# Kernel optimization log

Measured on AMD Instinct MI355X. Metric: run time of the kernel, lower is better.

## Reference

```python
import jax, jax.numpy as jnp
import numpy as np

DATA = 2048   # data_size / hidden_size
WIDTH = 4096  # width_size
T = 1000      # len(ts)


def setup_inputs() -> dict:
    key = jax.random.key(0)
    ks = jax.random.split(key, 10)
    # ts: evenly spaced times; small dt keeps 1000 Euler steps stable
    ts = jnp.arange(T, dtype=jnp.float32) * 1e-3
    y0 = jax.random.normal(ks[0], (DATA,), dtype=jnp.float32)
    def lin(k, fan_out, fan_in):
        kw, kb = jax.random.split(k)
        s = 1.0 / np.sqrt(fan_in)
        W = jax.random.uniform(kw, (fan_out, fan_in), jnp.float32, -s, s)
        b = jax.random.uniform(kb, (fan_out,), jnp.float32, -s, s)
        return W, b
    # eqx.nn.MLP(depth=3): in->w, w->w, w->w, w->out, softplus on all but last
    W0, b0 = lin(ks[1], WIDTH, DATA)
    W1, b1 = lin(ks[2], WIDTH, WIDTH)
    W2, b2 = lin(ks[3], WIDTH, WIDTH)
    W3, b3 = lin(ks[4], DATA, WIDTH)
    return {"ts": ts, "y0": y0, "W0": W0, "b0": b0, "W1": W1, "b1": b1,
            "W2": W2, "b2": b2, "W3": W3, "b3": b3}


def reference(ts, y0, W0, b0, W1, b1, W2, b2, W3, b3):
    dt = ts[1] - ts[0]

    def mlp(y):
        h = jax.nn.softplus(W0 @ y + b0)
        h = jax.nn.softplus(W1 @ h + b1)
        h = jax.nn.softplus(W2 @ h + b2)
        return W3 @ h + b3

    def step(y, _):
        y1 = y + dt * mlp(y)  # Euler step: y + dt * f(t, y)
        return y1, y1

    _, ys = jax.lax.scan(step, y0, None, length=ts.shape[0])
    return ys  # [T, DATA]
```

## Files before the change

### kernel.cpp

```cpp
#include <hip/hip_runtime.h>

#define NWG   256
#define TPB_R 256
#define TPB_S 1024
#define NSTEP 1000
#define NDATA 2048
#define WIDTH 4096

typedef __attribute__((ext_vector_type(4))) float f32x4;
typedef __attribute__((ext_vector_type(2))) float f32x2;
typedef __attribute__((ext_vector_type(2))) unsigned int u32x2;
typedef __attribute__((ext_vector_type(4))) unsigned int u32x4;
typedef unsigned int uint;

#define SCHED_FENCE() __builtin_amdgcn_sched_barrier(0)


__device__ __forceinline__ float sp_f(float v) {
  return fmaxf(v, 0.0f) + log1pf(expf(-fabsf(v)));
}

__device__ __forceinline__ float wred(float v) {
#pragma unroll
  for (int m = 32; m > 0; m >>= 1) v += __shfl_xor(v, m, 64);
  return v;
}


__device__ __forceinline__ void wait_vm0()   { asm volatile("s_waitcnt vmcnt(0)" ::: "memory"); SCHED_FENCE(); }
template<int N>
__device__ __forceinline__ void wait_vmN()   { asm volatile("s_waitcnt vmcnt(%0)" :: "n"(N) : "memory"); SCHED_FENCE(); }
__device__ __forceinline__ void wait_lgkm0() { asm volatile("s_waitcnt lgkmcnt(0)" ::: "memory"); SCHED_FENCE(); }
__device__ __forceinline__ void wgbar()      { __builtin_amdgcn_s_barrier(); SCHED_FENCE(); }


__device__ __forceinline__ void st_sc_x1(float* p, float v) {
  asm volatile("global_store_dword %0, %1, off sc0 sc1" :: "v"(p), "v"(v) : "memory");
}
__device__ __forceinline__ void st_sc_x2(float* p, f32x2 v) {
  asm volatile("global_store_dwordx2 %0, %1, off sc0 sc1" :: "v"(p), "v"(v) : "memory");
}
__device__ __forceinline__ void st_sc_x4(float* p, f32x4 v) {
  asm volatile("global_store_dwordx4 %0, %1, off sc0 sc1" :: "v"(p), "v"(v) : "memory");
}
__device__ __forceinline__ void ld_sc_x2_issue(const float* p, f32x2& v) {
  asm volatile("global_load_dwordx2 %0, %1, off sc0 sc1" : "=v"(v) : "v"(p) : "memory");
}
__device__ __forceinline__ void ld_sc_x4_issue(const f32x4* p, f32x4& v) {
  asm volatile("global_load_dwordx4 %0, %1, off sc0 sc1" : "=v"(v) : "v"(p) : "memory");
}
__device__ __forceinline__ void ld_sc_x1_issue(const float* p, float& v) {
  asm volatile("global_load_dword %0, %1, off sc0 sc1" : "=v"(v) : "v"(p) : "memory");
}
__device__ __forceinline__ uint ld_sc_u32(const uint* p) {
  uint v;
  asm volatile("global_load_dword %0, %1, off sc0 sc1\n\ts_waitcnt vmcnt(0)"
               : "=v"(v) : "v"(p) : "memory");
  return v;
}
__device__ __forceinline__ void st_sc_u32(uint* p, uint v) {
  asm volatile("global_store_dword %0, %1, off sc0 sc1" :: "v"(p), "v"(v) : "memory");
}

__device__ __forceinline__ void ld_g(const u32x4* p, u32x4& v) {
  asm volatile("global_load_dwordx4 %0, %1, off" : "=v"(v) : "v"(p) : "memory");
}


__device__ __forceinline__ void sync_stage_4096(uint* flags, uint tag, int wg,
                                                int tid, const float* src,
                                                float* xs) {
  wgbar();
  if (tid == 0) st_sc_u32(flags + wg * 16, tag);
  const uint* fp = flags + tid * 16;
  if (ld_sc_u32(fp) < tag) {
    do { __builtin_amdgcn_s_sleep(1); } while (ld_sc_u32(fp) < tag);
  }
  const f32x4* s = (const f32x4*)src + tid * 4;
  f32x4 a, b, c, d;
  ld_sc_x4_issue(s + 0, a); ld_sc_x4_issue(s + 1, b);
  ld_sc_x4_issue(s + 2, c); ld_sc_x4_issue(s + 3, d);
  wait_vm0();
  f32x4* l = (f32x4*)xs + tid * 4;
  l[0] = a; l[1] = b; l[2] = c; l[3] = d;
  wait_lgkm0();
  wgbar();
}

__device__ __forceinline__ void sync_stage_2048(uint* flags, uint tag, int wg,
                                                int tid, const float* src,
                                                float* xs) {
  wgbar();
  if (tid == 0) st_sc_u32(flags + wg * 16, tag);
  const uint* fp = flags + tid * 16;
  if (ld_sc_u32(fp) < tag) {
    do { __builtin_amdgcn_s_sleep(1); } while (ld_sc_u32(fp) < tag);
  }
  const f32x4* s = (const f32x4*)src + tid * 2;
  f32x4 a, b;
  ld_sc_x4_issue(s + 0, a); ld_sc_x4_issue(s + 1, b);
  wait_vm0();
  f32x4* l = (f32x4*)xs + tid * 2;
  l[0] = a; l[1] = b;
  wait_lgkm0();
  wgbar();
}


__device__ __forceinline__ uint bfr(float f) {
  uint u = __float_as_uint(f);
  return (u + 0x7fffu + ((u >> 16) & 1u)) >> 16;
}

__global__ void cvt_perm(const float* __restrict__ in, u32x4* __restrict__ out,
                         int rows, int K) {
  int idx = blockIdx.x * 256 + threadIdx.x;
  int cpr = K >> 3;
  if (idx >= rows * cpr) return;
  int row = idx / cpr, c = idx - row * cpr;
  int j = c >> 6, lane = c & 63;
  const f32x4* p = (const f32x4*)(in + (size_t)row * K + j * 512 + lane * 4);
  f32x4 lo = p[0];
  f32x4 hi = p[64];
  u32x4 o;
  o.x = bfr(lo.x) | (bfr(lo.y) << 16);
  o.y = bfr(lo.z) | (bfr(lo.w) << 16);
  o.z = bfr(hi.x) | (bfr(hi.y) << 16);
  o.w = bfr(hi.z) | (bfr(hi.w) << 16);
  out[idx] = o;
}


#define QF(Q, s) do{                                                 \
  s = fmaf(__uint_as_float((Q).x << 16),         xa.x, s);           \
  s = fmaf(__uint_as_float((Q).x & 0xffff0000u), xa.y, s);           \
  s = fmaf(__uint_as_float((Q).y << 16),         xa.z, s);           \
  s = fmaf(__uint_as_float((Q).y & 0xffff0000u), xa.w, s);           \
  s = fmaf(__uint_as_float((Q).z << 16),         xb.x, s);           \
  s = fmaf(__uint_as_float((Q).z & 0xffff0000u), xb.y, s);           \
  s = fmaf(__uint_as_float((Q).w << 16),         xb.z, s);           \
  s = fmaf(__uint_as_float((Q).w & 0xffff0000u), xb.w, s);           \
}while(0)

#define DC(Q, j, s) do{                                              \
  f32x4 xa = x4[(j)*128 + lane];                                     \
  f32x4 xb = x4[(j)*128 + 64 + lane];                                \
  QF(Q, s);                                                          \
}while(0)

#define DL4(j) do{                                                   \
  f32x4 xa = x4[(j)*128 + lane];                                     \
  f32x4 xb = x4[(j)*128 + 64 + lane];                                \
  u32x4 Q0 = w1p[0*512 + (j)*64 + lane];                             \
  u32x4 Q1 = w1p[1*512 + (j)*64 + lane];                             \
  u32x4 Q2 = w1p[2*512 + (j)*64 + lane];                             \
  u32x4 Q3 = w1p[3*512 + (j)*64 + lane];                             \
  QF(Q0, s0); QF(Q1, s1); QF(Q2, s2); QF(Q3, s3);                    \
}while(0)

#define DR4(j, Qa, Qb, Qc, Qd) do{                                   \
  f32x4 xa = x4[(j)*128 + lane];                                     \
  f32x4 xb = x4[(j)*128 + 64 + lane];                                \
  QF(Qa, s0); QF(Qb, s1); QF(Qc, s2); QF(Qd, s3);                    \
}while(0)

#define DR2(j, Qa, Qb) do{                                           \
  f32x4 xa = x4[(j)*128 + lane];                                     \
  f32x4 xb = x4[(j)*128 + 64 + lane];                                \
  QF(Qa, s0); QF(Qb, s1);                                            \
}while(0)

#define SREG(x) __int_as_float(__builtin_amdgcn_readfirstlane(__float_as_int(x)))


__global__ void __launch_bounds__(TPB_R, 1) ode_res(
    const float* __restrict__ ts, const float* __restrict__ y0,
    const u32x4* __restrict__ W0p, const float* __restrict__ b0,
    const u32x4* __restrict__ W1p, const float* __restrict__ b1,
    const u32x4* __restrict__ W2p, const float* __restrict__ b2,
    const u32x4* __restrict__ W3p, const float* __restrict__ b3,
    float* __restrict__ out, float* hA, float* hB,
    uint* flags)
{
  __shared__ u32x4 W1lds[16 * 512];
  __shared__ float xs[WIDTH];
  const int wg = blockIdx.x, tid = threadIdx.x;
  const int wave = tid >> 6, lane = tid & 63;
  const float dt = ts[1] - ts[0];
  const int rw = wg * 16 + wave * 4;
  const int rf = wg * 8 + wave * 2;
  const f32x4* x4 = (const f32x4*)xs;
  const u32x4* w1p = &W1lds[(wave * 4) * 512];

#pragma unroll
  for (int k = 0; k < 32; ++k)
    W1lds[k * 256 + tid] = W1p[(size_t)wg * 8192 + k * 256 + tid];

#define L2W(r,j) W2p[(size_t)(rw+(r))*512 + (j)*64 + lane]
  u32x4 C00=L2W(0,0),C01=L2W(0,1),C02=L2W(0,2),C03=L2W(0,3),C04=L2W(0,4),C05=L2W(0,5),C06=L2W(0,6),C07=L2W(0,7);
  u32x4 C10=L2W(1,0),C11=L2W(1,1),C12=L2W(1,2),C13=L2W(1,3),C14=L2W(1,4),C15=L2W(1,5),C16=L2W(1,6),C17=L2W(1,7);
  u32x4 C20=L2W(2,0),C21=L2W(2,1),C22=L2W(2,2),C23=L2W(2,3),C24=L2W(2,4),C25=L2W(2,5),C26=L2W(2,6),C27=L2W(2,7);
  u32x4 C30=L2W(3,0),C31=L2W(3,1),C32=L2W(3,2),C33=L2W(3,3),C34=L2W(3,4),C35=L2W(3,5),C36=L2W(3,6),C37=L2W(3,7);
#define L3W(r,j) W3p[(size_t)(rf+(r))*512 + (j)*64 + lane]
  u32x4 D00=L3W(0,0),D01=L3W(0,1),D02=L3W(0,2),D03=L3W(0,3),D04=L3W(0,4),D05=L3W(0,5),D06=L3W(0,6),D07=L3W(0,7);
  u32x4 D10=L3W(1,0),D11=L3W(1,1),D12=L3W(1,2),D13=L3W(1,3),D14=L3W(1,4),D15=L3W(1,5),D16=L3W(1,6),D17=L3W(1,7);

  const float b00=SREG(b0[rw]), b01=SREG(b0[rw+1]), b02=SREG(b0[rw+2]), b03=SREG(b0[rw+3]);
  const float b10=SREG(b1[rw]), b11=SREG(b1[rw+1]), b12=SREG(b1[rw+2]), b13=SREG(b1[rw+3]);
  const float b20=SREG(b2[rw]), b21=SREG(b2[rw+1]), b22=SREG(b2[rw+2]), b23=SREG(b2[rw+3]);
  const float b30=SREG(b3[rf]), b31=SREG(b3[rf+1]);

  wait_vm0(); wait_lgkm0();
  wgbar();

  const u32x4* w0base = W0p + (size_t)rw * 256 + lane;
#define ISSW0(r, Qa, Qb, Qc, Qd) do{ const u32x4* p_ = w0base + (size_t)(r)*256; \
  ld_g(p_, Qa); ld_g(p_+64, Qb); ld_g(p_+128, Qc); ld_g(p_+192, Qd); }while(0)

  u32x4 E0a,E0b,E0c,E0d, E1a,E1b,E1c,E1d, E2a,E2b,E2c,E2d, E3a,E3b,E3c,E3d;
  ISSW0(0, E0a,E0b,E0c,E0d);

  uint tag = 0;
  const float* yin = y0;
  for (int step = 0; step < NSTEP; ++step) {
    float s0, s1, s2, s3;
    sync_stage_2048(flags, tag, wg, tid, yin, xs); ++tag;
    ISSW0(1, E1a,E1b,E1c,E1d);
    s0 = 0.f; DC(E0a,0,s0); DC(E0b,1,s0); DC(E0c,2,s0); DC(E0d,3,s0);
    ISSW0(2, E2a,E2b,E2c,E2d);
    wait_vmN<4>();
    s1 = 0.f; DC(E1a,0,s1); DC(E1b,1,s1); DC(E1c,2,s1); DC(E1d,3,s1);
    ISSW0(3, E3a,E3b,E3c,E3d);
    wait_vmN<4>();
    s2 = 0.f; DC(E2a,0,s2); DC(E2b,1,s2); DC(E2c,2,s2); DC(E2d,3,s2);
    wait_vm0();
    s3 = 0.f; DC(E3a,0,s3); DC(E3b,1,s3); DC(E3c,2,s3); DC(E3d,3,s3);
    s0 = wred(s0); s1 = wred(s1); s2 = wred(s2); s3 = wred(s3);
    if (lane == 0) {
      f32x4 v; v.x = sp_f(s0+b00); v.y = sp_f(s1+b01); v.z = sp_f(s2+b02); v.w = sp_f(s3+b03);
      st_sc_x4(hA + rw, v);
    }
    wait_vm0();

    sync_stage_4096(flags, tag, wg, tid, hA, xs); ++tag;
    s0=0.f; s1=0.f; s2=0.f; s3=0.f;
    DL4(0); DL4(1); DL4(2); DL4(3); DL4(4); DL4(5); DL4(6); DL4(7);
    s0 = wred(s0); s1 = wred(s1); s2 = wred(s2); s3 = wred(s3);
    if (lane == 0) {
      f32x4 v; v.x = sp_f(s0+b10); v.y = sp_f(s1+b11); v.z = sp_f(s2+b12); v.w = sp_f(s3+b13);
      st_sc_x4(hB + rw, v);
    }
    wait_vm0();

    sync_stage_4096(flags, tag, wg, tid, hB, xs); ++tag;
    s0=0.f; s1=0.f; s2=0.f; s3=0.f;
    DR4(0, C00, C10, C20, C30); DR4(1, C01, C11, C21, C31);
    DR4(2, C02, C12, C22, C32); DR4(3, C03, C13, C23, C33);
    DR4(4, C04, C14, C24, C34); DR4(5, C05, C15, C25, C35);
    DR4(6, C06, C16, C26, C36); DR4(7, C07, C17, C27, C37);
    s0 = wred(s0); s1 = wred(s1); s2 = wred(s2); s3 = wred(s3);
    if (lane == 0) {
      f32x4 v; v.x = sp_f(s0+b20); v.y = sp_f(s1+b21); v.z = sp_f(s2+b22); v.w = sp_f(s3+b23);
      st_sc_x4(hA + rw, v);
    }
    wait_vm0();

    sync_stage_4096(flags, tag, wg, tid, hA, xs); ++tag;
    f32x2 yo;
    ld_sc_x2_issue(yin + rf, yo);
    s0=0.f; s1=0.f;
    DR2(0, D00, D10); DR2(1, D01, D11); DR2(2, D02, D12); DR2(3, D03, D13);
    DR2(4, D04, D14); DR2(5, D05, D15); DR2(6, D06, D16); DR2(7, D07, D17);
    s0 = wred(s0); s1 = wred(s1);
    wait_vm0();
    float* yout = out + (size_t)step * NDATA;
    if (lane == 0) {
      f32x2 v; v.x = yo.x + dt * (s0 + b30); v.y = yo.y + dt * (s1 + b31);
      st_sc_x2(yout + rf, v);
    }
    ISSW0(0, E0a,E0b,E0c,E0d);
    wait_vmN<4>();
    yin = yout;
  }
}


__device__ __forceinline__ void gbar1k(uint* flags, uint tag, int wg, int tid) {
  wgbar();
  if (tid == 0) st_sc_u32(flags + wg * 16, tag);
  if (tid < NWG) {
    const uint* fp = flags + tid * 16;
    if (ld_sc_u32(fp) < tag) {
      do { __builtin_amdgcn_s_sleep(1); } while (ld_sc_u32(fp) < tag);
    }
  }
  wgbar();
}

__device__ __forceinline__ void stage4096_1k(const float* src, float* xs, int tid) {
  f32x4 a;
  ld_sc_x4_issue((const f32x4*)src + tid, a);
  wait_vm0();
  ((f32x4*)xs)[tid] = a;
  wait_lgkm0();
  wgbar();
}
__device__ __forceinline__ void stage2048_1k(const float* src, float* xs, int tid) {
  f32x4 a;
  bool act = tid < 512;
  if (act) ld_sc_x4_issue((const f32x4*)src + tid, a);
  wait_vm0();
  if (act) ((f32x4*)xs)[tid] = a;
  wait_lgkm0();
  wgbar();
}

__device__ __forceinline__ void issue_row_f32(const float* W, size_t elemidx, int lane, f32x4* wr, int ni) {
  const f32x4* p = (const f32x4*)(W + elemidx) + lane;
  for (int i = 0; i < ni; ++i)
    asm volatile("global_load_dwordx4 %0, %1, off" : "=v"(wr[i]) : "v"(p + i * 64) : "memory");
}

template<int NI>
__device__ __forceinline__ float dot_row_f32(const f32x4* wr, const float* xs, int xoff, int lane) {
  const f32x4* x4 = (const f32x4*)xs + xoff;
  float a = 0.f;
#pragma unroll
  for (int i = 0; i < NI; ++i) {
    f32x4 xv = x4[i * 64 + lane];
    a = fmaf(wr[i].x, xv.x, a); a = fmaf(wr[i].y, xv.y, a);
    a = fmaf(wr[i].z, xv.z, a); a = fmaf(wr[i].w, xv.w, a);
  }
  return a;
}

__global__ void __launch_bounds__(TPB_S, 1) ode_stream(
    const float* __restrict__ ts, const float* __restrict__ y0,
    const float* __restrict__ W0, const float* __restrict__ b0,
    const float* __restrict__ W1, const float* __restrict__ b1,
    const float* __restrict__ W2, const float* __restrict__ b2,
    const float* __restrict__ W3, const float* __restrict__ b3,
    float* __restrict__ out, float* hA, float* hB,
    uint* flags)
{
  __shared__ float xs[WIDTH];
  __shared__ float ps[16];
  const int wg = blockIdx.x, tid = threadIdx.x;
  const int wave = tid >> 6, lane = tid & 63;
  const float dt = ts[1] - ts[0];
  const int rw = wg * 16 + wave;
  const int rF = wg * 8 + (wave >> 1);
  const int hf = wave & 1;

  f32x4 w0r[8], w1r[16], w2r[16], w3r[8];
  issue_row_f32(W0, (size_t)rw * NDATA, lane, w0r, 8);

  uint tag = 0;
  const float* yin = y0;
  for (int step = 0; step < NSTEP; ++step) {
    stage2048_1k(yin, xs, tid);
    float a = wred(dot_row_f32<8>(w0r, xs, 0, lane));
    if (lane == 0) st_sc_x1(hA + rw, sp_f(a + b0[rw]));
    issue_row_f32(W1, (size_t)rw * WIDTH, lane, w1r, 16);
    wait_vmN<16>();
    gbar1k(flags, ++tag, wg, tid);

    stage4096_1k(hA, xs, tid);
    a = wred(dot_row_f32<16>(w1r, xs, 0, lane));
    if (lane == 0) st_sc_x1(hB + rw, sp_f(a + b1[rw]));
    issue_row_f32(W2, (size_t)rw * WIDTH, lane, w2r, 16);
    wait_vmN<16>();
    gbar1k(flags, ++tag, wg, tid);

    stage4096_1k(hB, xs, tid);
    a = wred(dot_row_f32<16>(w2r, xs, 0, lane));
    if (lane == 0) st_sc_x1(hA + rw, sp_f(a + b2[rw]));
    issue_row_f32(W3, (size_t)rF * WIDTH + (size_t)hf * 2048, lane, w3r, 8);
    wait_vmN<8>();
    gbar1k(flags, ++tag, wg, tid);

    stage4096_1k(hA, xs, tid);
    float yo;
    ld_sc_x1_issue(yin + rF, yo);
    a = wred(dot_row_f32<8>(w3r, xs, hf * 512, lane));
    if (lane == 0) ps[wave] = a;
    wait_lgkm0();
    wgbar();
    wait_vm0();
    float* yout = out + (size_t)step * NDATA;
    if (hf == 0 && lane == 0) {
      float tot = ps[wave] + ps[wave + 1];
      st_sc_x1(yout + rF, yo + dt * (tot + b3[rF]));
    }
    issue_row_f32(W0, (size_t)rw * NDATA, lane, w0r, 8);
    wait_vmN<8>();
    gbar1k(flags, ++tag, wg, tid);
    yin = yout;
  }
}


#define WS_HA   0
#define WS_HB   16384
#define WS_CNT  32768
#define WS_WB   65536
static const size_t N_W0 = (size_t)WIDTH * NDATA;
static const size_t N_W1 = (size_t)WIDTH * WIDTH;
static const size_t N_W3 = (size_t)NDATA * WIDTH;

extern "C" void kernel_launch(void* const* d_in, const int* in_sizes, int n_in,
                              void* d_out, int out_size, void* d_ws, size_t ws_size,
                              hipStream_t stream) {
  const float* ts = (const float*)d_in[0];
  const float* y0 = (const float*)d_in[1];
  const float* W0 = (const float*)d_in[2];
  const float* b0 = (const float*)d_in[3];
  const float* W1 = (const float*)d_in[4];
  const float* b1 = (const float*)d_in[5];
  const float* W2 = (const float*)d_in[6];
  const float* b2 = (const float*)d_in[7];
  const float* W3 = (const float*)d_in[8];
  const float* b3 = (const float*)d_in[9];
  float* out = (float*)d_out;

  char* ws = (char*)d_ws;
  float* hA    = (float*)(ws + WS_HA);
  float* hB    = (float*)(ws + WS_HB);
  uint*  flags = (uint*)(ws + WS_CNT);

  hipMemsetAsync(ws + WS_CNT, 0, 16384, stream);

  const size_t need = WS_WB + (N_W0 + 2 * N_W1 + N_W3) * 2;
  if (ws_size >= need) {
    u32x4* W0p = (u32x4*)(ws + WS_WB);
    u32x4* W1p = W0p + N_W0 / 8;
    u32x4* W2p = W1p + N_W1 / 8;
    u32x4* W3p = W2p + N_W1 / 8;
    hipLaunchKernelGGL(cvt_perm, dim3((unsigned)(N_W0 / 8 / 256)), dim3(256), 0, stream, W0, W0p, WIDTH, NDATA);
    hipLaunchKernelGGL(cvt_perm, dim3((unsigned)(N_W1 / 8 / 256)), dim3(256), 0, stream, W1, W1p, WIDTH, WIDTH);
    hipLaunchKernelGGL(cvt_perm, dim3((unsigned)(N_W1 / 8 / 256)), dim3(256), 0, stream, W2, W2p, WIDTH, WIDTH);
    hipLaunchKernelGGL(cvt_perm, dim3((unsigned)(N_W3 / 8 / 256)), dim3(256), 0, stream, W3, W3p, NDATA, WIDTH);
    hipLaunchKernelGGL(ode_res, dim3(NWG), dim3(TPB_R), 0, stream,
                       ts, y0, W0p, b0, W1p, b1, W2p, b2, W3p, b3,
                       out, hA, hB, flags);
  } else {
    hipLaunchKernelGGL(ode_stream, dim3(NWG), dim3(TPB_S), 0, stream,
                       ts, y0, W0, b0, W1, b1, W2, b2, W3, b3,
                       out, hA, hB, flags);
  }
}
```

Before: 22.07 ms.

## Store activations as packed bf16 and use v_dot2 bf16 dot products

Hidden activations and the state vector are now rounded to bf16 and packed in pairs before being exchanged through global memory and staged in LDS. The matvec inner loop replaces the per-element unpack and FMA sequence with v_dot2_f32_bf16 instructions, which consume packed weight and activation pairs. This halves the traffic in the inter-workgroup exchange and the LDS footprint, and cuts ALU work in the dot products. The cost is lower precision on activations, including the ODE state fed to the first layer, which may accumulate error over the 1000 Euler steps.

```diff
diff --git a/kernel.cpp b/kernel.cpp
--- a/kernel.cpp
+++ b/kernel.cpp
@@ -26,6 +26,12 @@
   return v;
 }
 
+__device__ __forceinline__ uint pk_bf16(float lo, float hi) {
+  uint r;
+  asm("v_cvt_pk_bf16_f32 %0, %1, %2" : "=v"(r) : "v"(lo), "v"(hi));
+  return r;
+}
+
 
 __device__ __forceinline__ void wait_vm0()   { asm volatile("s_waitcnt vmcnt(0)" ::: "memory"); SCHED_FENCE(); }
 template<int N>
@@ -40,13 +46,16 @@
 __device__ __forceinline__ void st_sc_x2(float* p, f32x2 v) {
   asm volatile("global_store_dwordx2 %0, %1, off sc0 sc1" :: "v"(p), "v"(v) : "memory");
 }
-__device__ __forceinline__ void st_sc_x4(float* p, f32x4 v) {
-  asm volatile("global_store_dwordx4 %0, %1, off sc0 sc1" :: "v"(p), "v"(v) : "memory");
+__device__ __forceinline__ void st_sc_u2(uint* p, u32x2 v) {
+  asm volatile("global_store_dwordx2 %0, %1, off sc0 sc1" :: "v"(p), "v"(v) : "memory");
 }
 __device__ __forceinline__ void ld_sc_x2_issue(const float* p, f32x2& v) {
   asm volatile("global_load_dwordx2 %0, %1, off sc0 sc1" : "=v"(v) : "v"(p) : "memory");
 }
 __device__ __forceinline__ void ld_sc_x4_issue(const f32x4* p, f32x4& v) {
+  asm volatile("global_load_dwordx4 %0, %1, off sc0 sc1" : "=v"(v) : "v"(p) : "memory");
+}
+__device__ __forceinline__ void ld_sc_u4_issue(const u32x4* p, u32x4& v) {
   asm volatile("global_load_dwordx4 %0, %1, off sc0 sc1" : "=v"(v) : "v"(p) : "memory");
 }
 __device__ __forceinline__ void ld_sc_x1_issue(const float* p, float& v) {
@@ -67,29 +76,28 @@
 }
 
 
-__device__ __forceinline__ void sync_stage_4096(uint* flags, uint tag, int wg,
-                                                int tid, const float* src,
-                                                float* xs) {
+__device__ __forceinline__ void sync_stage_h(uint* flags, uint tag, int wg,
+                                             int tid, const uint* src,
+                                             uint* xs) {
   wgbar();
   if (tid == 0) st_sc_u32(flags + wg * 16, tag);
   const uint* fp = flags + tid * 16;
   if (ld_sc_u32(fp) < tag) {
     do { __builtin_amdgcn_s_sleep(1); } while (ld_sc_u32(fp) < tag);
   }
-  const f32x4* s = (const f32x4*)src + tid * 4;
-  f32x4 a, b, c, d;
-  ld_sc_x4_issue(s + 0, a); ld_sc_x4_issue(s + 1, b);
-  ld_sc_x4_issue(s + 2, c); ld_sc_x4_issue(s + 3, d);
+  const u32x4* s = (const u32x4*)src + tid * 2;
+  u32x4 a, b;
+  ld_sc_u4_issue(s + 0, a); ld_sc_u4_issue(s + 1, b);
   wait_vm0();
-  f32x4* l = (f32x4*)xs + tid * 4;
-  l[0] = a; l[1] = b; l[2] = c; l[3] = d;
+  u32x4* l = (u32x4*)xs + tid * 2;
+  l[0] = a; l[1] = b;
   wait_lgkm0();
   wgbar();
 }
 
-__device__ __forceinline__ void sync_stage_2048(uint* flags, uint tag, int wg,
-                                                int tid, const float* src,
-                                                float* xs) {
+__device__ __forceinline__ void sync_stage_y(uint* flags, uint tag, int wg,
+                                             int tid, const float* src,
+                                             uint* xs) {
   wgbar();
   if (tid == 0) st_sc_u32(flags + wg * 16, tag);
   const uint* fp = flags + tid * 16;
@@ -100,8 +108,10 @@
   f32x4 a, b;
   ld_sc_x4_issue(s + 0, a); ld_sc_x4_issue(s + 1, b);
   wait_vm0();
-  f32x4* l = (f32x4*)xs + tid * 2;
-  l[0] = a; l[1] = b;
+  u32x4 o;
+  o.x = pk_bf16(a.x, a.y); o.y = pk_bf16(a.z, a.w);
+  o.z = pk_bf16(b.x, b.y); o.w = pk_bf16(b.z, b.w);
+  ((u32x4*)xs)[tid] = o;
   wait_lgkm0();
   wgbar();
 }
@@ -131,26 +141,22 @@
 }
 
 
+#define VD(W, X, s) asm("v_dot2_f32_bf16 %0, %1, %2, %0" : "+v"(s) : "v"(W), "v"(X))
+
 #define QF(Q, s) do{                                                 \
-  s = fmaf(__uint_as_float((Q).x << 16),         xa.x, s);           \
-  s = fmaf(__uint_as_float((Q).x & 0xffff0000u), xa.y, s);           \
-  s = fmaf(__uint_as_float((Q).y << 16),         xa.z, s);           \
-  s = fmaf(__uint_as_float((Q).y & 0xffff0000u), xa.w, s);           \
-  s = fmaf(__uint_as_float((Q).z << 16),         xb.x, s);           \
-  s = fmaf(__uint_as_float((Q).z & 0xffff0000u), xb.y, s);           \
-  s = fmaf(__uint_as_float((Q).w << 16),         xb.z, s);           \
-  s = fmaf(__uint_as_float((Q).w & 0xffff0000u), xb.w, s);           \
+  VD((Q).x, xa2.x, s); VD((Q).y, xa2.y, s);                          \
+  VD((Q).z, xb2.x, s); VD((Q).w, xb2.y, s);                          \
 }while(0)
 
 #define DC(Q, j, s) do{                                              \
-  f32x4 xa = x4[(j)*128 + lane];                                     \
-  f32x4 xb = x4[(j)*128 + 64 + lane];                                \
+  u32x2 xa2 = xw2[(j)*128 + lane];                                   \
+  u32x2 xb2 = xw2[(j)*128 + 64 + lane];                              \
   QF(Q, s);                                                          \
 }while(0)
 
 #define DL4(j) do{                                                   \
-  f32x4 xa = x4[(j)*128 + lane];                                     \
-  f32x4 xb = x4[(j)*128 + 64 + lane];                                \
+  u32x2 xa2 = xw2[(j)*128 + lane];                                   \
+  u32x2 xb2 = xw2[(j)*128 + 64 + lane];                              \
   u32x4 Q0 = w1p[0*512 + (j)*64 + lane];                             \
   u32x4 Q1 = w1p[1*512 + (j)*64 + lane];                             \
   u32x4 Q2 = w1p[2*512 + (j)*64 + lane];                             \
@@ -159,14 +165,14 @@
 }while(0)
 
 #define DR4(j, Qa, Qb, Qc, Qd) do{                                   \
-  f32x4 xa = x4[(j)*128 + lane];                                     \
-  f32x4 xb = x4[(j)*128 + 64 + lane];                                \
+  u32x2 xa2 = xw2[(j)*128 + lane];                                   \
+  u32x2 xb2 = xw2[(j)*128 + 64 + lane];                              \
   QF(Qa, s0); QF(Qb, s1); QF(Qc, s2); QF(Qd, s3);                    \
 }while(0)
 
 #define DR2(j, Qa, Qb) do{                                           \
-  f32x4 xa = x4[(j)*128 + lane];                                     \
-  f32x4 xb = x4[(j)*128 + 64 + lane];                                \
+  u32x2 xa2 = xw2[(j)*128 + lane];                                   \
+  u32x2 xb2 = xw2[(j)*128 + 64 + lane];                              \
   QF(Qa, s0); QF(Qb, s1);                                            \
 }while(0)
 
@@ -179,17 +185,17 @@
     const u32x4* __restrict__ W1p, const float* __restrict__ b1,
     const u32x4* __restrict__ W2p, const float* __restrict__ b2,
     const u32x4* __restrict__ W3p, const float* __restrict__ b3,
-    float* __restrict__ out, float* hA, float* hB,
+    float* __restrict__ out, uint* hA, uint* hB,
     uint* flags)
 {
   __shared__ u32x4 W1lds[16 * 512];
-  __shared__ float xs[WIDTH];
+  __shared__ uint xs[2048];
   const int wg = blockIdx.x, tid = threadIdx.x;
   const int wave = tid >> 6, lane = tid & 63;
   const float dt = ts[1] - ts[0];
   const int rw = wg * 16 + wave * 4;
   const int rf = wg * 8 + wave * 2;
-  const f32x4* x4 = (const f32x4*)xs;
+  const u32x2* xw2 = (const u32x2*)xs;
   const u32x4* w1p = &W1lds[(wave * 4) * 512];
 
 #pragma unroll
@@ -224,7 +230,7 @@
   const float* yin = y0;
   for (int step = 0; step < NSTEP; ++step) {
     float s0, s1, s2, s3;
-    sync_stage_2048(flags, tag, wg, tid, yin, xs); ++tag;
+    sync_stage_y(flags, tag, wg, tid, yin, xs); ++tag;
     ISSW0(1, E1a,E1b,E1c,E1d);
     s0 = 0.f; DC(E0a,0,s0); DC(E0b,1,s0); DC(E0c,2,s0); DC(E0d,3,s0);
     ISSW0(2, E2a,E2b,E2c,E2d);
@@ -237,22 +243,24 @@
     s3 = 0.f; DC(E3a,0,s3); DC(E3b,1,s3); DC(E3c,2,s3); DC(E3d,3,s3);
     s0 = wred(s0); s1 = wred(s1); s2 = wred(s2); s3 = wred(s3);
     if (lane == 0) {
-      f32x4 v; v.x = sp_f(s0+b00); v.y = sp_f(s1+b01); v.z = sp_f(s2+b02); v.w = sp_f(s3+b03);
-      st_sc_x4(hA + rw, v);
-    }
-    wait_vm0();
-
-    sync_stage_4096(flags, tag, wg, tid, hA, xs); ++tag;
+      u32x2 v; v.x = pk_bf16(sp_f(s0+b00), sp_f(s1+b01));
+               v.y = pk_bf16(sp_f(s2+b02), sp_f(s3+b03));
+      st_sc_u2(hA + (rw >> 1), v);
+    }
+    wait_vm0();
+
+    sync_stage_h(flags, tag, wg, tid, hA, xs); ++tag;
     s0=0.f; s1=0.f; s2=0.f; s3=0.f;
     DL4(0); DL4(1); DL4(2); DL4(3); DL4(4); DL4(5); DL4(6); DL4(7);
     s0 = wred(s0); s1 = wred(s1); s2 = wred(s2); s3 = wred(s3);
     if (lane == 0) {
-      f32x4 v; v.x = sp_f(s0+b10); v.y = sp_f(s1+b11); v.z = sp_f(s2+b12); v.w = sp_f(s3+b13);
-      st_sc_x4(hB + rw, v);
-    }
-    wait_vm0();
-
-    sync_stage_4096(flags, tag, wg, tid, hB, xs); ++tag;
+      u32x2 v; v.x = pk_bf16(sp_f(s0+b10), sp_f(s1+b11));
+               v.y = pk_bf16(sp_f(s2+b12), sp_f(s3+b13));
+      st_sc_u2(hB + (rw >> 1), v);
+    }
+    wait_vm0();
+
+    sync_stage_h(flags, tag, wg, tid, hB, xs); ++tag;
     s0=0.f; s1=0.f; s2=0.f; s3=0.f;
     DR4(0, C00, C10, C20, C30); DR4(1, C01, C11, C21, C31);
     DR4(2, C02, C12, C22, C32); DR4(3, C03, C13, C23, C33);
@@ -260,12 +268,13 @@
     DR4(6, C06, C16, C26, C36); DR4(7, C07, C17, C27, C37);
     s0 = wred(s0); s1 = wred(s1); s2 = wred(s2); s3 = wred(s3);
     if (lane == 0) {
-      f32x4 v; v.x = sp_f(s0+b20); v.y = sp_f(s1+b21); v.z = sp_f(s2+b22); v.w = sp_f(s3+b23);
-      st_sc_x4(hA + rw, v);
-    }
-    wait_vm0();
-
-    sync_stage_4096(flags, tag, wg, tid, hA, xs); ++tag;
+      u32x2 v; v.x = pk_bf16(sp_f(s0+b20), sp_f(s1+b21));
+               v.y = pk_bf16(sp_f(s2+b22), sp_f(s3+b23));
+      st_sc_u2(hA + (rw >> 1), v);
+    }
+    wait_vm0();
+
+    sync_stage_h(flags, tag, wg, tid, hA, xs); ++tag;
     f32x2 yo;
     ld_sc_x2_issue(yin + rf, yo);
     s0=0.f; s1=0.f;
@@ -424,8 +433,6 @@
   float* out = (float*)d_out;
 
   char* ws = (char*)d_ws;
-  float* hA    = (float*)(ws + WS_HA);
-  float* hB    = (float*)(ws + WS_HB);
   uint*  flags = (uint*)(ws + WS_CNT);
 
   hipMemsetAsync(ws + WS_CNT, 0, 16384, stream);
@@ -436,6 +443,8 @@
     u32x4* W1p = W0p + N_W0 / 8;
     u32x4* W2p = W1p + N_W1 / 8;
     u32x4* W3p = W2p + N_W1 / 8;
+    uint* hA = (uint*)(ws + WS_HA);
+    uint* hB = (uint*)(ws + WS_HB);
     hipLaunchKernelGGL(cvt_perm, dim3((unsigned)(N_W0 / 8 / 256)), dim3(256), 0, stream, W0, W0p, WIDTH, NDATA);
     hipLaunchKernelGGL(cvt_perm, dim3((unsigned)(N_W1 / 8 / 256)), dim3(256), 0, stream, W1, W1p, WIDTH, WIDTH);
     hipLaunchKernelGGL(cvt_perm, dim3((unsigned)(N_W1 / 8 / 256)), dim3(256), 0, stream, W2, W2p, WIDTH, WIDTH);
@@ -444,8 +453,10 @@
                        ts, y0, W0p, b0, W1p, b1, W2p, b2, W3p, b3,
                        out, hA, hB, flags);
   } else {
+    float* hAf = (float*)(ws + WS_HA);
+    float* hBf = (float*)(ws + WS_HB);
     hipLaunchKernelGGL(ode_stream, dim3(NWG), dim3(TPB_S), 0, stream,
                        ts, y0, W0, b0, W1, b1, W2, b2, W3, b3,
-                       out, hA, hB, flags);
-  }
-}
+                       out, hAf, hBf, flags);
+  }
+}
```

After: 19.87 ms. 1.11x faster.
